# Performance work log

Hardware: AMD Instinct MI355X
Metric: run time of the kernel (lower is better)

The kernel has to match this reference:

```python
import jax, jax.numpy as jnp
import numpy as np

B, D, L, NH = 8, 1024, 1024, 8
DK = D // NH  # = Dv = 128
NEG = -1e30


def setup_inputs() -> dict:
    key = jax.random.key(0)
    kx, km, kq, kk, kv, ko = jax.random.split(key, 6)
    x = jax.random.normal(kx, (B, D, L), dtype=jnp.float32)
    # binary mask over sequence positions (float, as in the torch code)
    mask = (jax.random.uniform(km, (B, L)) > 0.1).astype(jnp.float32)
    # xavier-ish scale for per-head projections, kaiming-ish for Wo
    s_qkv = np.sqrt(2.0 / (D + DK)).astype(np.float32)
    Wq = jax.random.normal(kq, (NH, D, DK), dtype=jnp.float32) * s_qkv
    Wk = jax.random.normal(kk, (NH, D, DK), dtype=jnp.float32) * s_qkv
    Wv = jax.random.normal(kv, (NH, D, DK), dtype=jnp.float32) * s_qkv
    Wo = jax.random.normal(ko, (D, DK * NH), dtype=jnp.float32) * np.sqrt(2.0 / D).astype(np.float32)
    return {"x": x, "mask": mask, "Wq": Wq, "Wk": Wk, "Wv": Wv, "Wo": Wo}


def reference(x, mask, Wq, Wk, Wv, Wo):
    # x: [B, D, L] -> [B, L, D]
    xt = jnp.swapaxes(x, 1, 2)
    scale = 1.0 / np.sqrt(DK).astype(np.float32)
    # batched per-head projections (equivalent to the per-head loop)
    q = jnp.einsum("bld,hdk->bhlk", xt, Wq)  # [B,H,L,Dk]
    k = jnp.einsum("bld,hdk->bhlk", xt, Wk)
    v = jnp.einsum("bld,hdk->bhlk", xt, Wv)
    # scores[b,h,q_pos,k_pos]
    scores = jnp.einsum("bhqd,bhkd->bhqk", q, k) * scale
    # mask.unsqueeze(2) in torch -> additive mask along the QUERY axis
    scores = scores + (1.0 - mask)[:, None, :, None] * NEG
    # faithful quirk: softmax over dim=1 of [B,Lq,Lk] == query axis (axis=2 here)
    attn = jax.nn.softmax(scores, axis=2)
    heads = jnp.einsum("bhqk,bhkd->bhqd", attn, v)  # [B,H,L,Dv]
    head = jnp.swapaxes(heads, 1, 2).reshape(B, L, NH * DK)  # concat heads
    out = head @ Wo  # [B, L, D]
    return jnp.swapaxes(out, 1, 2)  # [B, D, L]
```

## Files before the change

### kernel.cpp

```cpp
#include <hip/hip_runtime.h>

typedef short bf16x8 __attribute__((ext_vector_type(8)));
typedef float f32x4 __attribute__((ext_vector_type(4)));

#define MASK_NEG (-1e30f)

__device__ __forceinline__ unsigned short f2bf(float f) {
  union { float f; unsigned u; } v; v.f = f;
  unsigned r = v.u + 0x7fffu + ((v.u >> 16) & 1u);
  return (unsigned short)(r >> 16);
}

__device__ __forceinline__ void gl_lds16(const void* g, void* l) {
  __builtin_amdgcn_global_load_lds(
      (__attribute__((address_space(1))) void*)(void*)g,
      (__attribute__((address_space(3))) void*)l, 16, 0, 0);
}

__device__ __forceinline__ void transpose_tile(
    const float* __restrict__ s, unsigned short* __restrict__ d,
    int R, int C, int x0, int y0, int t, float tile[64][65]) {
  {
    const int r = t >> 4, c4 = (t & 15) * 4;
    for (int it = 0; it < 4; ++it) {
      const int rr = r + it * 16;
      const float4 v = *(const float4*)(s + (size_t)(y0 + rr) * C + x0 + c4);
      tile[rr][c4 + 0] = v.x; tile[rr][c4 + 1] = v.y;
      tile[rr][c4 + 2] = v.z; tile[rr][c4 + 3] = v.w;
    }
  }
  __syncthreads();
  {
    const int cc = t >> 4, r4 = (t & 15) * 4;
    for (int it = 0; it < 4; ++it) {
      const int c = cc + it * 16;
      ushort4 o;
      o.x = f2bf(tile[r4 + 0][c]); o.y = f2bf(tile[r4 + 1][c]);
      o.z = f2bf(tile[r4 + 2][c]); o.w = f2bf(tile[r4 + 3][c]);
      *(ushort4*)(d + (size_t)(x0 + c) * R + y0 + r4) = o;
    }
  }
}

__global__ __launch_bounds__(256) void transpose_x_wo(
    const float* __restrict__ x, const float* __restrict__ Wo,
    unsigned short* __restrict__ xt, unsigned short* __restrict__ Wot) {
  __shared__ float tile[64][65];
  const int z = blockIdx.z;
  const float* s = (z < 8) ? (x + (size_t)z * 1048576) : Wo;
  unsigned short* d = (z < 8) ? (xt + (size_t)z * 1048576) : Wot;
  transpose_tile(s, d, 1024, 1024, blockIdx.x * 64, blockIdx.y * 64,
                 threadIdx.x, tile);
}

__global__ __launch_bounds__(256) void transpose_w24(
    const float* __restrict__ Wq, const float* __restrict__ Wk,
    const float* __restrict__ Wv, unsigned short* __restrict__ WqkvT) {
  __shared__ float tile[64][65];
  const int z = blockIdx.z;
  const int sel = z >> 3, h = z & 7;
  const float* base = (sel == 0) ? Wq : (sel == 1) ? Wk : Wv;
  const float* s = base + (size_t)h * 131072;
  unsigned short* d = WqkvT + (size_t)z * 131072;
  transpose_tile(s, d, 1024, 128, blockIdx.x * 64, blockIdx.y * 64,
                 threadIdx.x, tile);
}

template<bool F32OUT>
__global__ __launch_bounds__(256) void gemm_tn(
    const unsigned short* __restrict__ A, const unsigned short* __restrict__ B,
    void* __restrict__ Cv,
    int K, int ldA, int ldB, int ldC, float scale,
    long sAl, long sAb, long sAh,
    long sBl, long sBb, long sBh,
    long sCl, long sCb, long sCh,
    int zbase, int zdiv, unsigned short* __restrict__ Vt)
{
  __shared__ unsigned short As[128 * 64];
  __shared__ unsigned short Bs[128 * 64];
  int bx, by, bz;
  {
    const int nx = gridDim.x, ny = gridDim.y;
    const int nwg = nx * ny * gridDim.z;
    int flat = blockIdx.x + nx * (blockIdx.y + ny * blockIdx.z);
    if ((nwg & 7) == 0) flat = (flat & 7) * (nwg >> 3) + (flat >> 3);
    bx = flat % nx; flat /= nx;
    by = flat % ny; bz = flat / ny;
  }
  const int z = bz;
  const int g = zbase + z;
  const int gb = g / zdiv, gh = g % zdiv;
  const unsigned short* Ab = A + (size_t)z * sAl + (size_t)gb * sAb + (size_t)gh * sAh;
  const unsigned short* Bb = B + (size_t)z * sBl + (size_t)gb * sBb + (size_t)gh * sBh;
  const int m0 = by * 128, n0 = bx * 128;
  const int t = threadIdx.x;
  const int lane = t & 63;
  const int wave = t >> 6;
  const int wm = wave >> 1, wn = wave & 1;

  const int sr2 = t >> 3;
  const int ss8 = t & 7;
  const int sq8 = ss8 ^ (sr2 & 7);

  const unsigned short* ap0 = Ab + (size_t)(m0 +  0 + sr2) * ldA + sq8 * 8;
  const unsigned short* ap1 = Ab + (size_t)(m0 + 32 + sr2) * ldA + sq8 * 8;
  const unsigned short* ap2 = Ab + (size_t)(m0 + 64 + sr2) * ldA + sq8 * 8;
  const unsigned short* ap3 = Ab + (size_t)(m0 + 96 + sr2) * ldA + sq8 * 8;
  const unsigned short* bp0 = Bb + (size_t)(n0 +  0 + sr2) * ldB + sq8 * 8;
  const unsigned short* bp1 = Bb + (size_t)(n0 + 32 + sr2) * ldB + sq8 * 8;
  const unsigned short* bp2 = Bb + (size_t)(n0 + 64 + sr2) * ldB + sq8 * 8;
  const unsigned short* bp3 = Bb + (size_t)(n0 + 96 + sr2) * ldB + sq8 * 8;

  char* asd0 = (char*)As +     0 + t * 16;
  char* asd1 = (char*)As +  4096 + t * 16;
  char* asd2 = (char*)As +  8192 + t * 16;
  char* asd3 = (char*)As + 12288 + t * 16;
  char* bsd0 = (char*)Bs +     0 + t * 16;
  char* bsd1 = (char*)Bs +  4096 + t * 16;
  char* bsd2 = (char*)Bs +  8192 + t * 16;
  char* bsd3 = (char*)Bs + 12288 + t * 16;

  const int tq = lane & 15, qd = lane >> 4;

  f32x4 acc[4][4];
  #pragma unroll
  for (int i = 0; i < 4; ++i)
    #pragma unroll
    for (int j = 0; j < 4; ++j)
      acc[i][j] = f32x4{0.f, 0.f, 0.f, 0.f};

  const int kIters = K >> 6;
  for (int kt = 0; kt < kIters; ++kt) {
    __syncthreads();
    gl_lds16(ap0, asd0); gl_lds16(ap1, asd1);
    gl_lds16(ap2, asd2); gl_lds16(ap3, asd3);
    gl_lds16(bp0, bsd0); gl_lds16(bp1, bsd1);
    gl_lds16(bp2, bsd2); gl_lds16(bp3, bsd3);
    ap0 += 64; ap1 += 64; ap2 += 64; ap3 += 64;
    bp0 += 64; bp1 += 64; bp2 += 64; bp3 += 64;
    __builtin_amdgcn_s_waitcnt(0x0f70);
    __syncthreads();

    #pragma unroll
    for (int kk = 0; kk < 2; ++kk) {
      bf16x8 af[4], bfr[4];
      #pragma unroll
      for (int i = 0; i < 4; ++i) {
        const int R = wm * 64 + i * 16 + tq;
        const int slot = (kk * 4 + qd) ^ (R & 7);
        af[i] = *(const bf16x8*)(As + R * 64 + slot * 8);
      }
      #pragma unroll
      for (int j = 0; j < 4; ++j) {
        const int R = wn * 64 + j * 16 + tq;
        const int slot = (kk * 4 + qd) ^ (R & 7);
        bfr[j] = *(const bf16x8*)(Bs + R * 64 + slot * 8);
      }
      #pragma unroll
      for (int i = 0; i < 4; ++i)
        #pragma unroll
        for (int j = 0; j < 4; ++j)
          acc[i][j] = __builtin_amdgcn_mfma_f32_16x16x32_bf16(af[i], bfr[j], acc[i][j], 0, 0, 0);
    }
  }

  if (!F32OUT && Vt != nullptr && gh >= 16) {
    unsigned short* Vb = Vt + (size_t)(gb * 8 + (gh - 16)) * 131072;
    #pragma unroll
    for (int i = 0; i < 4; ++i) {
      const int row = m0 + wm * 64 + i * 16 + qd * 4;
      #pragma unroll
      for (int j = 0; j < 4; ++j) {
        const int col = n0 + wn * 64 + j * 16 + tq;
        ushort4 o;
        o.x = f2bf(acc[i][j][0] * scale);
        o.y = f2bf(acc[i][j][1] * scale);
        o.z = f2bf(acc[i][j][2] * scale);
        o.w = f2bf(acc[i][j][3] * scale);
        *(ushort4*)(Vb + (size_t)col * 1024 + row) = o;
      }
    }
    return;
  }

  const size_t cOff = (size_t)z * sCl + (size_t)gb * sCb + (size_t)gh * sCh;
  #pragma unroll
  for (int i = 0; i < 4; ++i) {
    const int row = m0 + wm * 64 + i * 16 + qd * 4;
    #pragma unroll
    for (int j = 0; j < 4; ++j) {
      const int col = n0 + wn * 64 + j * 16 + tq;
      if constexpr (F32OUT) {
        float* C = (float*)Cv + cOff;
        #pragma unroll
        for (int rr = 0; rr < 4; ++rr)
          C[(size_t)(row + rr) * ldC + col] = acc[i][j][rr] * scale;
      } else {
        unsigned short* C = (unsigned short*)Cv + cOff;
        #pragma unroll
        for (int rr = 0; rr < 4; ++rr)
          C[(size_t)(row + rr) * ldC + col] = f2bf(acc[i][j][rr] * scale);
      }
    }
  }
}

__global__ __launch_bounds__(256, 2) void scores_colsum(
    const unsigned short* __restrict__ QKV, float* __restrict__ colsum,
    const float* __restrict__ mask)
{
  __shared__ unsigned short lds[24576];
  unsigned short* Qs = lds;

  const int bid = blockIdx.x;
  const int w = ((bid & 7) << 6) | (bid >> 3);
  const int g = w >> 3, qx = w & 7;
  const int b = g >> 3, h = g & 7;
  const unsigned short* Qg = QKV + (size_t)b * 3145728 + (size_t)h * 131072
                                 + (size_t)qx * 16384;
  const unsigned short* Kg = QKV + (size_t)b * 3145728 + (size_t)(8 + h) * 131072;

  const int t = threadIdx.x;
  const int lane = t & 63, wave = t >> 6;
  const int wm = wave >> 1, wn = wave & 1;
  const int tq = lane & 15, qd = lane >> 4;

  #pragma unroll
  for (int it = 0; it < 8; ++it) {
    const int c = it * 256 + t;
    const int row = c >> 4;
    const int src = (c ^ (c >> 4)) & 15;
    gl_lds16(Qg + (size_t)row * 128 + src * 8, (char*)Qs + c * 16);
  }
  #pragma unroll
  for (int it = 0; it < 4; ++it) {
    const int c = it * 256 + t;
    const int row = c >> 4;
    const int src = (c ^ (c >> 4)) & 15;
    gl_lds16(Kg + (size_t)row * 128 + src * 8, (char*)(lds + 16384) + c * 16);
  }
  __builtin_amdgcn_s_waitcnt(0x0f70);
  __syncthreads();

  bf16x8 qf[4][4];
  #pragma unroll
  for (int i = 0; i < 4; ++i) {
    const int R = wm * 64 + i * 16 + tq;
    #pragma unroll
    for (int kk = 0; kk < 4; ++kk)
      qf[i][kk] = *(const bf16x8*)(Qs + R * 128 + (((kk * 4 + qd) ^ (R & 15)) * 8));
  }
  __syncthreads();

  const float scl = 0.08838834764831845f;
  float aq[4][4];
  {
    const float* mrow = mask + (size_t)b * 1024 + qx * 128;
    #pragma unroll
    for (int i = 0; i < 4; ++i) {
      const float4 m4 = *(const float4*)(mrow + wm * 64 + i * 16 + qd * 4);
      aq[i][0] = (1.f - m4.x) * MASK_NEG - 20.f;
      aq[i][1] = (1.f - m4.y) * MASK_NEG - 20.f;
      aq[i][2] = (1.f - m4.z) * MASK_NEG - 20.f;
      aq[i][3] = (1.f - m4.w) * MASK_NEG - 20.f;
    }
  }
  float* cs = colsum + (size_t)g * 1024;

  for (int kt = 0; kt < 16; ++kt) {
    __syncthreads();
    if (kt < 15) {
      unsigned short* Kn = ((kt + 1) & 1) ? lds : (lds + 16384);
      const unsigned short* Kgn = Kg + (size_t)(kt + 1) * 64 * 128;
      #pragma unroll
      for (int it = 0; it < 4; ++it) {
        const int c = it * 256 + t;
        const int row = c >> 4;
        const int src = (c ^ (c >> 4)) & 15;
        gl_lds16(Kgn + (size_t)row * 128 + src * 8, (char*)Kn + c * 16);
      }
      __builtin_amdgcn_s_waitcnt(0x0f74);
    } else {
      __builtin_amdgcn_s_waitcnt(0x0f70);
    }
    __syncthreads();

    const unsigned short* Kc = (kt & 1) ? lds : (lds + 16384);
    f32x4 acc_s[4][2];
    #pragma unroll
    for (int i = 0; i < 4; ++i)
      #pragma unroll
      for (int j = 0; j < 2; ++j)
        acc_s[i][j] = f32x4{0.f, 0.f, 0.f, 0.f};
    #pragma unroll
    for (int kk = 0; kk < 4; ++kk) {
      bf16x8 kf[2];
      #pragma unroll
      for (int j = 0; j < 2; ++j) {
        const int R = wn * 32 + j * 16 + tq;
        kf[j] = *(const bf16x8*)(Kc + R * 128 + (((kk * 4 + qd) ^ (R & 15)) * 8));
      }
      #pragma unroll
      for (int i = 0; i < 4; ++i)
        #pragma unroll
        for (int j = 0; j < 2; ++j)
          acc_s[i][j] = __builtin_amdgcn_mfma_f32_16x16x32_bf16(qf[i][kk], kf[j], acc_s[i][j], 0, 0, 0);
    }

    float cp0 = 0.f, cp1 = 0.f;
    #pragma unroll
    for (int i = 0; i < 4; ++i)
      #pragma unroll
      for (int rr = 0; rr < 4; ++rr) {
        cp0 += __expf(acc_s[i][0][rr] * scl + aq[i][rr]);
        cp1 += __expf(acc_s[i][1][rr] * scl + aq[i][rr]);
      }
    cp0 += __shfl_xor(cp0, 16, 64); cp0 += __shfl_xor(cp0, 32, 64);
    cp1 += __shfl_xor(cp1, 16, 64); cp1 += __shfl_xor(cp1, 32, 64);
    if (qd == 0) {
      atomicAdd(&cs[kt * 64 + wn * 32 + tq], cp0);
      atomicAdd(&cs[kt * 64 + wn * 32 + 16 + tq], cp1);
    }
  }
}

__global__ __launch_bounds__(256, 2) void attn_pv_fused(
    const unsigned short* __restrict__ QKV, const unsigned short* __restrict__ Vp,
    unsigned short* __restrict__ Hp, const float* __restrict__ mask,
    const float* __restrict__ colsum)
{
  __shared__ unsigned short lds[40960];
  unsigned short* Ps = lds;
  unsigned short* Qs = lds;

  const int bid = blockIdx.x;
  const int w = ((bid & 7) << 6) | (bid >> 3);
  const int g = w >> 3, qx = w & 7;
  const int b = g >> 3, h = g & 7;
  const unsigned short* Qg = QKV + (size_t)b * 3145728 + (size_t)h * 131072
                                 + (size_t)qx * 16384;
  const unsigned short* Kg = QKV + (size_t)b * 3145728 + (size_t)(8 + h) * 131072;
  const unsigned short* Vg = Vp + (size_t)g * 131072;

  const int t = threadIdx.x;
  const int lane = t & 63, wave = t >> 6;
  const int wm = wave >> 1, wn = wave & 1;
  const int tq = lane & 15, qd = lane >> 4;

  #pragma unroll
  for (int it = 0; it < 8; ++it) {
    const int c = it * 256 + t;
    const int row = c >> 4;
    const int src = (c ^ (c >> 4)) & 15;
    gl_lds16(Qg + (size_t)row * 128 + src * 8, (char*)Qs + c * 16);
  }
  #pragma unroll
  for (int it = 0; it < 4; ++it) {
    const int c = it * 256 + t;
    const int row = c >> 4;
    const int src = (c ^ (c >> 4)) & 15;
    gl_lds16(Kg + (size_t)row * 128 + src * 8, (char*)(lds + 16384) + c * 16);
  }
  #pragma unroll
  for (int it = 0; it < 4; ++it) {
    const int c = it * 256 + t;
    const int row = c >> 3;
    const int src = (c ^ (c >> 3)) & 7;
    gl_lds16(Vg + (size_t)row * 1024 + src * 8, (char*)(lds + 24576) + c * 16);
  }
  __builtin_amdgcn_s_waitcnt(0x0f70);
  __syncthreads();

  bf16x8 qf[4][4];
  #pragma unroll
  for (int i = 0; i < 4; ++i) {
    const int R = wm * 64 + i * 16 + tq;
    #pragma unroll
    for (int kk = 0; kk < 4; ++kk)
      qf[i][kk] = *(const bf16x8*)(Qs + R * 128 + (((kk * 4 + qd) ^ (R & 15)) * 8));
  }
  __syncthreads();

  f32x4 acc_h[4][4];
  #pragma unroll
  for (int i = 0; i < 4; ++i)
    #pragma unroll
    for (int j = 0; j < 4; ++j)
      acc_h[i][j] = f32x4{0.f, 0.f, 0.f, 0.f};

  const float scl = 0.08838834764831845f;
  float aq[4][4];
  {
    const float* mrow = mask + (size_t)b * 1024 + qx * 128;
    #pragma unroll
    for (int i = 0; i < 4; ++i) {
      const float4 m4 = *(const float4*)(mrow + wm * 64 + i * 16 + qd * 4);
      aq[i][0] = (1.f - m4.x) * MASK_NEG - 20.f;
      aq[i][1] = (1.f - m4.y) * MASK_NEG - 20.f;
      aq[i][2] = (1.f - m4.z) * MASK_NEG - 20.f;
      aq[i][3] = (1.f - m4.w) * MASK_NEG - 20.f;
    }
  }
  const float* cs = colsum + (size_t)g * 1024;

  for (int kt = 0; kt < 16; ++kt) {
    __syncthreads();
    if (kt < 15) {
      unsigned short* Kn = ((kt + 1) & 1) ? (lds + 8192) : (lds + 16384);
      unsigned short* Vn = ((kt + 1) & 1) ? (lds + 32768) : (lds + 24576);
      const unsigned short* Kgn = Kg + (size_t)(kt + 1) * 64 * 128;
      #pragma unroll
      for (int it = 0; it < 4; ++it) {
        const int c = it * 256 + t;
        const int row = c >> 4;
        const int src = (c ^ (c >> 4)) & 15;
        gl_lds16(Kgn + (size_t)row * 128 + src * 8, (char*)Kn + c * 16);
      }
      #pragma unroll
      for (int it = 0; it < 4; ++it) {
        const int c = it * 256 + t;
        const int row = c >> 3;
        const int src = (c ^ (c >> 3)) & 7;
        gl_lds16(Vg + (size_t)row * 1024 + (kt + 1) * 64 + src * 8, (char*)Vn + c * 16);
      }
      __builtin_amdgcn_s_waitcnt(0x0f78);
    } else {
      __builtin_amdgcn_s_waitcnt(0x0f70);
    }
    __syncthreads();

    const unsigned short* Kc = (kt & 1) ? (lds + 8192) : (lds + 16384);
    const unsigned short* Vc = (kt & 1) ? (lds + 32768) : (lds + 24576);

    f32x4 acc_s[4][2];
    #pragma unroll
    for (int i = 0; i < 4; ++i)
      #pragma unroll
      for (int j = 0; j < 2; ++j)
        acc_s[i][j] = f32x4{0.f, 0.f, 0.f, 0.f};
    #pragma unroll
    for (int kk = 0; kk < 4; ++kk) {
      bf16x8 kf[2];
      #pragma unroll
      for (int j = 0; j < 2; ++j) {
        const int R = wn * 32 + j * 16 + tq;
        kf[j] = *(const bf16x8*)(Kc + R * 128 + (((kk * 4 + qd) ^ (R & 15)) * 8));
      }
      #pragma unroll
      for (int i = 0; i < 4; ++i)
        #pragma unroll
        for (int j = 0; j < 2; ++j)
          acc_s[i][j] = __builtin_amdgcn_mfma_f32_16x16x32_bf16(qf[i][kk], kf[j], acc_s[i][j], 0, 0, 0);
    }

    const float rcs0 = 1.0f / cs[kt * 64 + wn * 32 + tq];
    const float rcs1 = 1.0f / cs[kt * 64 + wn * 32 + 16 + tq];
    #pragma unroll
    for (int i = 0; i < 4; ++i) {
      const int q0 = wm * 64 + i * 16 + qd * 4;
      #pragma unroll
      for (int rr = 0; rr < 4; ++rr) {
        const int q = q0 + rr;
        #pragma unroll
        for (int j = 0; j < 2; ++j) {
          const int kl = wn * 32 + j * 16 + tq;
          const float e = __expf(acc_s[i][j][rr] * scl + aq[i][rr]) * (j ? rcs1 : rcs0);
          Ps[q * 64 + ((((kl >> 3) ^ (q & 7)) * 8) | (kl & 7))] = f2bf(e);
        }
      }
    }
    __syncthreads();

    #pragma unroll
    for (int k2 = 0; k2 < 2; ++k2) {
      bf16x8 pf[4], vf[4];
      #pragma unroll
      for (int i = 0; i < 4; ++i) {
        const int R = wm * 64 + i * 16 + tq;
        pf[i] = *(const bf16x8*)(Ps + R * 64 + (((k2 * 4 + qd) ^ (R & 7)) * 8));
      }
      #pragma unroll
      for (int j = 0; j < 4; ++j) {
        const int R = wn * 64 + j * 16 + tq;
        vf[j] = *(const bf16x8*)(Vc + R * 64 + (((k2 * 4 + qd) ^ (R & 7)) * 8));
      }
      #pragma unroll
      for (int i = 0; i < 4; ++i)
        #pragma unroll
        for (int j = 0; j < 4; ++j)
          acc_h[i][j] = __builtin_amdgcn_mfma_f32_16x16x32_bf16(pf[i], vf[j], acc_h[i][j], 0, 0, 0);
    }
  }

  unsigned short* Hb = Hp + (size_t)b * 1048576 + (size_t)qx * 131072 + h * 128;
  #pragma unroll
  for (int i = 0; i < 4; ++i) {
    const int q0 = wm * 64 + i * 16 + qd * 4;
    #pragma unroll
    for (int j = 0; j < 4; ++j) {
      const int dv = wn * 64 + j * 16 + tq;
      #pragma unroll
      for (int rr = 0; rr < 4; ++rr)
        Hb[(size_t)(q0 + rr) * 1024 + dv] = f2bf(acc_h[i][j][rr]);
    }
  }
}

extern "C" void kernel_launch(void* const* d_in, const int* in_sizes, int n_in,
                              void* d_out, int out_size, void* d_ws, size_t ws_size,
                              hipStream_t stream) {
  const float* x    = (const float*)d_in[0];
  const float* mask = (const float*)d_in[1];
  const float* Wq   = (const float*)d_in[2];
  const float* Wk   = (const float*)d_in[3];
  const float* Wv   = (const float*)d_in[4];
  const float* Wo   = (const float*)d_in[5];
  float* out = (float*)d_out;

  char* p = (char*)d_ws;
  unsigned short* xt    = (unsigned short*)p; p += 16777216;
  unsigned short* WqkvT = (unsigned short*)p; p += 6291456;
  unsigned short* Wot   = (unsigned short*)p; p += 2097152;
  unsigned short* QKV   = (unsigned short*)p; p += 50331648;
  unsigned short* Vp    = (unsigned short*)p; p += 16777216;
  unsigned short* Hp    = (unsigned short*)p; p += 16777216;
  float* colsum = (float*)p; p += 262144;

  hipMemsetAsync(colsum, 0, 262144, stream);

  transpose_x_wo<<<dim3(16, 16, 9), 256, 0, stream>>>(x, Wo, xt, Wot);
  transpose_w24<<<dim3(2, 16, 24), 256, 0, stream>>>(Wq, Wk, Wv, WqkvT);

  gemm_tn<false><<<dim3(1, 8, 192), 256, 0, stream>>>(
      xt, WqkvT, (void*)QKV, 1024, 1024, 1024, 128, 1.f,
      0L, 1048576L, 0L,  0L, 0L, 131072L,  0L, 3145728L, 131072L, 0, 24, Vp);

  scores_colsum<<<dim3(512, 1, 1), 256, 0, stream>>>(QKV, colsum, mask);

  attn_pv_fused<<<dim3(512, 1, 1), 256, 0, stream>>>(QKV, Vp, Hp, mask, colsum);

  gemm_tn<true><<<dim3(8, 8, 8), 256, 0, stream>>>(
      Wot, Hp, (void*)out, 1024, 1024, 1024, 1024, 1.f,
      0L, 0L, 0L,  0L, 1048576L, 0L,  0L, 1048576L, 0L, 0, 1, nullptr);
}
```

Baseline: 285.2 us.

## Accumulate column sums in LDS and relax barrier waitcnts for deeper prefetch

In scores_colsum, per-tile column partial sums now go into a shared-memory buffer split by wave row, and each block flushes them with one coalesced atomicAdd pass at the end. This replaces many scattered global atomics issued inside the loop. Both kernels also swap __syncthreads for raw s_barrier plus explicit vmcnt waits, which lets the K/V prefetch for the next tile stay in flight across the barriers instead of draining. The hand-picked vmcnt values must match the number of outstanding loads exactly, so a miscount could read LDS before the data arrives.

```diff
diff --git a/kernel.cpp b/kernel.cpp
--- a/kernel.cpp
+++ b/kernel.cpp
@@ -210,6 +210,7 @@
     const float* __restrict__ mask)
 {
   __shared__ unsigned short lds[24576];
+  __shared__ float csacc[2][1024];
   unsigned short* Qs = lds;
 
   const int bid = blockIdx.x;
@@ -265,13 +266,12 @@
       aq[i][3] = (1.f - m4.w) * MASK_NEG - 20.f;
     }
   }
-  float* cs = colsum + (size_t)g * 1024;
 
   for (int kt = 0; kt < 16; ++kt) {
-    __syncthreads();
+    __builtin_amdgcn_s_barrier();
     if (kt < 15) {
       unsigned short* Kn = ((kt + 1) & 1) ? lds : (lds + 16384);
-      const unsigned short* Kgn = Kg + (size_t)(kt + 1) * 64 * 128;
+      const unsigned short* Kgn = Kg + (size_t)(kt + 1) * 8192;
       #pragma unroll
       for (int it = 0; it < 4; ++it) {
         const int c = it * 256 + t;
@@ -279,11 +279,11 @@
         const int src = (c ^ (c >> 4)) & 15;
         gl_lds16(Kgn + (size_t)row * 128 + src * 8, (char*)Kn + c * 16);
       }
-      __builtin_amdgcn_s_waitcnt(0x0f74);
+      asm volatile("s_waitcnt vmcnt(4)" ::: "memory");
     } else {
-      __builtin_amdgcn_s_waitcnt(0x0f70);
-    }
-    __syncthreads();
+      asm volatile("s_waitcnt vmcnt(0)" ::: "memory");
+    }
+    __builtin_amdgcn_s_barrier();
 
     const unsigned short* Kc = (kt & 1) ? lds : (lds + 16384);
     f32x4 acc_s[4][2];
@@ -318,9 +318,17 @@
     cp0 += __shfl_xor(cp0, 16, 64); cp0 += __shfl_xor(cp0, 32, 64);
     cp1 += __shfl_xor(cp1, 16, 64); cp1 += __shfl_xor(cp1, 32, 64);
     if (qd == 0) {
-      atomicAdd(&cs[kt * 64 + wn * 32 + tq], cp0);
-      atomicAdd(&cs[kt * 64 + wn * 32 + 16 + tq], cp1);
-    }
+      csacc[wm][kt * 64 + wn * 32 + tq] = cp0;
+      csacc[wm][kt * 64 + wn * 32 + 16 + tq] = cp1;
+    }
+  }
+
+  __syncthreads();
+  float* cs = colsum + (size_t)g * 1024;
+  #pragma unroll
+  for (int r = 0; r < 4; ++r) {
+    const int idx = r * 256 + t;
+    atomicAdd(&cs[idx], csacc[0][idx] + csacc[1][idx]);
   }
 }
 
@@ -404,11 +412,11 @@
   const float* cs = colsum + (size_t)g * 1024;
 
   for (int kt = 0; kt < 16; ++kt) {
-    __syncthreads();
+    __builtin_amdgcn_s_barrier();
     if (kt < 15) {
       unsigned short* Kn = ((kt + 1) & 1) ? (lds + 8192) : (lds + 16384);
       unsigned short* Vn = ((kt + 1) & 1) ? (lds + 32768) : (lds + 24576);
-      const unsigned short* Kgn = Kg + (size_t)(kt + 1) * 64 * 128;
+      const unsigned short* Kgn = Kg + (size_t)(kt + 1) * 8192;
       #pragma unroll
       for (int it = 0; it < 4; ++it) {
         const int c = it * 256 + t;
@@ -423,11 +431,11 @@
         const int src = (c ^ (c >> 3)) & 7;
         gl_lds16(Vg + (size_t)row * 1024 + (kt + 1) * 64 + src * 8, (char*)Vn + c * 16);
       }
-      __builtin_amdgcn_s_waitcnt(0x0f78);
+      asm volatile("s_waitcnt vmcnt(12)" ::: "memory");
     } else {
-      __builtin_amdgcn_s_waitcnt(0x0f70);
-    }
-    __syncthreads();
+      asm volatile("s_waitcnt vmcnt(4)" ::: "memory");
+    }
+    __builtin_amdgcn_s_barrier();
 
     const unsigned short* Kc = (kt & 1) ? (lds + 8192) : (lds + 16384);
     const unsigned short* Vc = (kt & 1) ? (lds + 32768) : (lds + 24576);
@@ -469,7 +477,11 @@
         }
       }
     }
-    __syncthreads();
+    if (kt < 15)
+      asm volatile("s_waitcnt vmcnt(8) lgkmcnt(0)" ::: "memory");
+    else
+      asm volatile("s_waitcnt vmcnt(0) lgkmcnt(0)" ::: "memory");
+    __builtin_amdgcn_s_barrier();
 
     #pragma unroll
     for (int k2 = 0; k2 < 2; ++k2) {
```

Result: faster. 277.5 us (-2.7%).

## Halve query tile per block, single-buffer K/V, and batch colsum atomics

Applied to the files above, without the earlier changes.

Both attention kernels now process 64 query rows per block instead of 128, launching twice as many blocks with launch bounds raised to 4 blocks per CU. K/V double buffering is dropped in favour of a single LDS buffer to cut LDS and register use. The colsum kernel accumulates per-tile column partials in shared memory and issues one atomic per column at the end instead of atomics every tile. MFMA sections are wrapped in s_setprio. The trade-off is that K/V loads are no longer overlapped with compute within a block, and each block now re-reads the full K (and V) for half as many queries, so that traffic doubles. The bet is that the extra occupancy hides the load latency.

```diff
diff --git a/kernel.cpp b/kernel.cpp
--- a/kernel.cpp
+++ b/kernel.cpp
@@ -205,19 +205,18 @@
   }
 }
 
-__global__ __launch_bounds__(256, 2) void scores_colsum(
+__global__ __launch_bounds__(256, 4) void scores_colsum(
     const unsigned short* __restrict__ QKV, float* __restrict__ colsum,
     const float* __restrict__ mask)
 {
-  __shared__ unsigned short lds[24576];
-  unsigned short* Qs = lds;
-
+  __shared__ unsigned short kbuf[8192];
+  __shared__ float csacc[2][1024];
   const int bid = blockIdx.x;
-  const int w = ((bid & 7) << 6) | (bid >> 3);
-  const int g = w >> 3, qx = w & 7;
+  const int w = ((bid & 7) << 7) | (bid >> 3);
+  const int g = w >> 4, qx = w & 15;
   const int b = g >> 3, h = g & 7;
   const unsigned short* Qg = QKV + (size_t)b * 3145728 + (size_t)h * 131072
-                                 + (size_t)qx * 16384;
+                                 + (size_t)qx * 8192;
   const unsigned short* Kg = QKV + (size_t)b * 3145728 + (size_t)(8 + h) * 131072;
 
   const int t = threadIdx.x;
@@ -226,90 +225,75 @@
   const int tq = lane & 15, qd = lane >> 4;
 
   #pragma unroll
-  for (int it = 0; it < 8; ++it) {
-    const int c = it * 256 + t;
-    const int row = c >> 4;
-    const int src = (c ^ (c >> 4)) & 15;
-    gl_lds16(Qg + (size_t)row * 128 + src * 8, (char*)Qs + c * 16);
-  }
-  #pragma unroll
   for (int it = 0; it < 4; ++it) {
     const int c = it * 256 + t;
     const int row = c >> 4;
     const int src = (c ^ (c >> 4)) & 15;
-    gl_lds16(Kg + (size_t)row * 128 + src * 8, (char*)(lds + 16384) + c * 16);
-  }
-  __builtin_amdgcn_s_waitcnt(0x0f70);
+    gl_lds16(Qg + (size_t)row * 128 + src * 8, (char*)kbuf + c * 16);
+  }
   __syncthreads();
 
-  bf16x8 qf[4][4];
-  #pragma unroll
-  for (int i = 0; i < 4; ++i) {
-    const int R = wm * 64 + i * 16 + tq;
+  bf16x8 qf[2][4];
+  #pragma unroll
+  for (int i = 0; i < 2; ++i) {
+    const int q = wm * 32 + i * 16 + tq;
     #pragma unroll
     for (int kk = 0; kk < 4; ++kk)
-      qf[i][kk] = *(const bf16x8*)(Qs + R * 128 + (((kk * 4 + qd) ^ (R & 15)) * 8));
+      qf[i][kk] = *(const bf16x8*)(kbuf + q * 128 + (((kk * 4 + qd) ^ (q & 15)) * 8));
   }
   __syncthreads();
 
   const float scl = 0.08838834764831845f;
-  float aq[4][4];
+  float aq[2][4];
   {
-    const float* mrow = mask + (size_t)b * 1024 + qx * 128;
-    #pragma unroll
-    for (int i = 0; i < 4; ++i) {
-      const float4 m4 = *(const float4*)(mrow + wm * 64 + i * 16 + qd * 4);
+    const float* mrow = mask + (size_t)b * 1024 + qx * 64;
+    #pragma unroll
+    for (int i = 0; i < 2; ++i) {
+      const float4 m4 = *(const float4*)(mrow + wm * 32 + i * 16 + qd * 4);
       aq[i][0] = (1.f - m4.x) * MASK_NEG - 20.f;
       aq[i][1] = (1.f - m4.y) * MASK_NEG - 20.f;
       aq[i][2] = (1.f - m4.z) * MASK_NEG - 20.f;
       aq[i][3] = (1.f - m4.w) * MASK_NEG - 20.f;
     }
   }
-  float* cs = colsum + (size_t)g * 1024;
 
   for (int kt = 0; kt < 16; ++kt) {
     __syncthreads();
-    if (kt < 15) {
-      unsigned short* Kn = ((kt + 1) & 1) ? lds : (lds + 16384);
-      const unsigned short* Kgn = Kg + (size_t)(kt + 1) * 64 * 128;
-      #pragma unroll
-      for (int it = 0; it < 4; ++it) {
-        const int c = it * 256 + t;
-        const int row = c >> 4;
-        const int src = (c ^ (c >> 4)) & 15;
-        gl_lds16(Kgn + (size_t)row * 128 + src * 8, (char*)Kn + c * 16);
-      }
-      __builtin_amdgcn_s_waitcnt(0x0f74);
-    } else {
-      __builtin_amdgcn_s_waitcnt(0x0f70);
-    }
-    __syncthreads();
-
-    const unsigned short* Kc = (kt & 1) ? lds : (lds + 16384);
-    f32x4 acc_s[4][2];
-    #pragma unroll
-    for (int i = 0; i < 4; ++i)
+    #pragma unroll
+    for (int it = 0; it < 4; ++it) {
+      const int c = it * 256 + t;
+      const int row = c >> 4;
+      const int src = (c ^ (c >> 4)) & 15;
+      gl_lds16(Kg + (size_t)(kt * 64 + row) * 128 + src * 8, (char*)kbuf + c * 16);
+    }
+    __syncthreads();
+
+    f32x4 acc_s[2][2];
+    #pragma unroll
+    for (int i = 0; i < 2; ++i)
       #pragma unroll
       for (int j = 0; j < 2; ++j)
         acc_s[i][j] = f32x4{0.f, 0.f, 0.f, 0.f};
+    __builtin_amdgcn_s_setprio(1);
     #pragma unroll
     for (int kk = 0; kk < 4; ++kk) {
       bf16x8 kf[2];
       #pragma unroll
       for (int j = 0; j < 2; ++j) {
-        const int R = wn * 32 + j * 16 + tq;
-        kf[j] = *(const bf16x8*)(Kc + R * 128 + (((kk * 4 + qd) ^ (R & 15)) * 8));
-      }
-      #pragma unroll
-      for (int i = 0; i < 4; ++i)
+        const int k = wn * 32 + j * 16 + tq;
+        kf[j] = *(const bf16x8*)(kbuf + k * 128 + (((kk * 4 + qd) ^ (k & 15)) * 8));
+      }
+      #pragma unroll
+      for (int i = 0; i < 2; ++i)
         #pragma unroll
         for (int j = 0; j < 2; ++j)
           acc_s[i][j] = __builtin_amdgcn_mfma_f32_16x16x32_bf16(qf[i][kk], kf[j], acc_s[i][j], 0, 0, 0);
     }
+    __builtin_amdgcn_s_setprio(0);
 
     float cp0 = 0.f, cp1 = 0.f;
     #pragma unroll
-    for (int i = 0; i < 4; ++i)
+    for (int i = 0; i < 2; ++i)
       #pragma unroll
       for (int rr = 0; rr < 4; ++rr) {
         cp0 += __expf(acc_s[i][0][rr] * scl + aq[i][rr]);
@@ -318,27 +302,36 @@
     cp0 += __shfl_xor(cp0, 16, 64); cp0 += __shfl_xor(cp0, 32, 64);
     cp1 += __shfl_xor(cp1, 16, 64); cp1 += __shfl_xor(cp1, 32, 64);
     if (qd == 0) {
-      atomicAdd(&cs[kt * 64 + wn * 32 + tq], cp0);
-      atomicAdd(&cs[kt * 64 + wn * 32 + 16 + tq], cp1);
-    }
-  }
-}
-
-__global__ __launch_bounds__(256, 2) void attn_pv_fused(
+      csacc[wm][kt * 64 + wn * 32 + tq] = cp0;
+      csacc[wm][kt * 64 + wn * 32 + 16 + tq] = cp1;
+    }
+  }
+
+  __syncthreads();
+  float* cs = colsum + (size_t)g * 1024;
+  #pragma unroll
+  for (int r = 0; r < 4; ++r) {
+    const int idx = r * 256 + t;
+    atomicAdd(&cs[idx], csacc[0][idx] + csacc[1][idx]);
+  }
+}
+
+__global__ __launch_bounds__(256, 4) void attn_pv_fused(
     const unsigned short* __restrict__ QKV, const unsigned short* __restrict__ Vp,
     unsigned short* __restrict__ Hp, const float* __restrict__ mask,
     const float* __restrict__ colsum)
 {
-  __shared__ unsigned short lds[40960];
+  __shared__ unsigned short lds[20480];
   unsigned short* Ps = lds;
-  unsigned short* Qs = lds;
+  unsigned short* Ks = lds + 4096;
+  unsigned short* Vs = lds + 12288;
 
   const int bid = blockIdx.x;
-  const int w = ((bid & 7) << 6) | (bid >> 3);
-  const int g = w >> 3, qx = w & 7;
+  const int w = ((bid & 7) << 7) | (bid >> 3);
+  const int g = w >> 4, qx = w & 15;
   const int b = g >> 3, h = g & 7;
   const unsigned short* Qg = QKV + (size_t)b * 3145728 + (size_t)h * 131072
-                                 + (size_t)qx * 16384;
+                                 + (size_t)qx * 8192;
   const unsigned short* Kg = QKV + (size_t)b * 3145728 + (size_t)(8 + h) * 131072;
   const unsigned short* Vg = Vp + (size_t)g * 131072;
 
@@ -348,53 +341,38 @@
   const int tq = lane & 15, qd = lane >> 4;
 
   #pragma unroll
-  for (int it = 0; it < 8; ++it) {
-    const int c = it * 256 + t;
-    const int row = c >> 4;
-    const int src = (c ^ (c >> 4)) & 15;
-    gl_lds16(Qg + (size_t)row * 128 + src * 8, (char*)Qs + c * 16);
-  }
-  #pragma unroll
   for (int it = 0; it < 4; ++it) {
     const int c = it * 256 + t;
     const int row = c >> 4;
     const int src = (c ^ (c >> 4)) & 15;
-    gl_lds16(Kg + (size_t)row * 128 + src * 8, (char*)(lds + 16384) + c * 16);
-  }
-  #pragma unroll
-  for (int it = 0; it < 4; ++it) {
-    const int c = it * 256 + t;
-    const int row = c >> 3;
-    const int src = (c ^ (c >> 3)) & 7;
-    gl_lds16(Vg + (size_t)row * 1024 + src * 8, (char*)(lds + 24576) + c * 16);
-  }
-  __builtin_amdgcn_s_waitcnt(0x0f70);
+    gl_lds16(Qg + (size_t)row * 128 + src * 8, (char*)Ks + c * 16);
+  }
   __syncthreads();
 
-  bf16x8 qf[4][4];
-  #pragma unroll
-  for (int i = 0; i < 4; ++i) {
-    const int R = wm * 64 + i * 16 + tq;
+  bf16x8 qf[2][4];
+  #pragma unroll
+  for (int i = 0; i < 2; ++i) {
+    const int q = wm * 32 + i * 16 + tq;
     #pragma unroll
     for (int kk = 0; kk < 4; ++kk)
-      qf[i][kk] = *(const bf16x8*)(Qs + R * 128 + (((kk * 4 + qd) ^ (R & 15)) * 8));
+      qf[i][kk] = *(const bf16x8*)(Ks + q * 128 + (((kk * 4 + qd) ^ (q & 15)) * 8));
   }
   __syncthreads();
 
-  f32x4 acc_h[4][4];
-  #pragma unroll
-  for (int i = 0; i < 4; ++i)
+  f32x4 acc_h[2][4];
+  #pragma unroll
+  for (int i = 0; i < 2; ++i)
     #pragma unroll
     for (int j = 0; j < 4; ++j)
       acc_h[i][j] = f32x4{0.f, 0.f, 0.f, 0.f};
 
   const float scl = 0.08838834764831845f;
-  float aq[4][4];
+  float aq[2][4];
   {
-    const float* mrow = mask + (size_t)b * 1024 + qx * 128;
-    #pragma unroll
-    for (int i = 0; i < 4; ++i) {
-      const float4 m4 = *(const float4*)(mrow + wm * 64 + i * 16 + qd * 4);
+    const float* mrow = mask + (size_t)b * 1024 + qx * 64;
+    #pragma unroll
+    for (int i = 0; i < 2; ++i) {
+      const float4 m4 = *(const float4*)(mrow + wm * 32 + i * 16 + qd * 4);
       aq[i][0] = (1.f - m4.x) * MASK_NEG - 20.f;
       aq[i][1] = (1.f - m4.y) * MASK_NEG - 20.f;
       aq[i][2] = (1.f - m4.z) * MASK_NEG - 20.f;
@@ -405,59 +383,50 @@
 
   for (int kt = 0; kt < 16; ++kt) {
     __syncthreads();
-    if (kt < 15) {
-      unsigned short* Kn = ((kt + 1) & 1) ? (lds + 8192) : (lds + 16384);
-      unsigned short* Vn = ((kt + 1) & 1) ? (lds + 32768) : (lds + 24576);
-      const unsigned short* Kgn = Kg + (size_t)(kt + 1) * 64 * 128;
-      #pragma unroll
-      for (int it = 0; it < 4; ++it) {
-        const int c = it * 256 + t;
-        const int row = c >> 4;
-        const int src = (c ^ (c >> 4)) & 15;
-        gl_lds16(Kgn + (size_t)row * 128 + src * 8, (char*)Kn + c * 16);
-      }
-      #pragma unroll
-      for (int it = 0; it < 4; ++it) {
-        const int c = it * 256 + t;
-        const int row = c >> 3;
-        const int src = (c ^ (c >> 3)) & 7;
-        gl_lds16(Vg + (size_t)row * 1024 + (kt + 1) * 64 + src * 8, (char*)Vn + c * 16);
-      }
-      __builtin_amdgcn_s_waitcnt(0x0f78);
-    } else {
-      __builtin_amdgcn_s_waitcnt(0x0f70);
-    }
-    __syncthreads();
-
-    const unsigned short* Kc = (kt & 1) ? (lds + 8192) : (lds + 16384);
-    const unsigned short* Vc = (kt & 1) ? (lds + 32768) : (lds + 24576);
-
-    f32x4 acc_s[4][2];
-    #pragma unroll
-    for (int i = 0; i < 4; ++i)
+    #pragma unroll
+    for (int it = 0; it < 4; ++it) {
+      const int c = it * 256 + t;
+      const int row = c >> 4;
+      const int src = (c ^ (c >> 4)) & 15;
+      gl_lds16(Kg + (size_t)(kt * 64 + row) * 128 + src * 8, (char*)Ks + c * 16);
+    }
+    #pragma unroll
+    for (int it = 0; it < 4; ++it) {
+      const int c = it * 256 + t;
+      const int row = c >> 3;
+      const int src = (c ^ (c >> 3)) & 7;
+      gl_lds16(Vg + (size_t)row * 1024 + kt * 64 + src * 8, (char*)Vs + c * 16);
+    }
+    const float rcs0 = 1.0f / cs[kt * 64 + wn * 32 + tq];
+    const float rcs1 = 1.0f / cs[kt * 64 + wn * 32 + 16 + tq];
+    __syncthreads();
+
+    f32x4 acc_s[2][2];
+    #pragma unroll
+    for (int i = 0; i < 2; ++i)
       #pragma unroll
       for (int j = 0; j < 2; ++j)
         acc_s[i][j] = f32x4{0.f, 0.f, 0.f, 0.f};
+    __builtin_amdgcn_s_setprio(1);
     #pragma unroll
     for (int kk = 0; kk < 4; ++kk) {
       bf16x8 kf[2];
       #pragma unroll
       for (int j = 0; j < 2; ++j) {
-        const int R = wn * 32 + j * 16 + tq;
-        kf[j] = *(const bf16x8*)(Kc + R * 128 + (((kk * 4 + qd) ^ (R & 15)) * 8));
-      }
-      #pragma unroll
-      for (int i = 0; i < 4; ++i)
+        const int k = wn * 32 + j * 16 + tq;
+        kf[j] = *(const bf16x8*)(Ks + k * 128 + (((kk * 4 + qd) ^ (k & 15)) * 8));
+      }
+      #pragma unroll
+      for (int i = 0; i < 2; ++i)
         #pragma unroll
         for (int j = 0; j < 2; ++j)
           acc_s[i][j] = __builtin_amdgcn_mfma_f32_16x16x32_bf16(qf[i][kk], kf[j], acc_s[i][j], 0, 0, 0);
     }
-
-    const float rcs0 = 1.0f / cs[kt * 64 + wn * 32 + tq];
-    const float rcs1 = 1.0f / cs[kt * 64 + wn * 32 + 16 + tq];
-    #pragma unroll
-    for (int i = 0; i < 4; ++i) {
-      const int q0 = wm * 64 + i * 16 + qd * 4;
+    __builtin_amdgcn_s_setprio(0);
+
+    #pragma unroll
+    for (int i = 0; i < 2; ++i) {
+      const int q0 = wm * 32 + i * 16 + qd * 4;
       #pragma unroll
       for (int rr = 0; rr < 4; ++rr) {
         const int q = q0 + rr;
@@ -465,37 +434,40 @@
         for (int j = 0; j < 2; ++j) {
           const int kl = wn * 32 + j * 16 + tq;
           const float e = __expf(acc_s[i][j][rr] * scl + aq[i][rr]) * (j ? rcs1 : rcs0);
-          Ps[q * 64 + ((((kl >> 3) ^ (q & 7)) * 8) | (kl & 7))] = f2bf(e);
+          Ps[q * 64 + (((kl >> 3) ^ (q & 7)) * 8) + (kl & 7)] = f2bf(e);
         }
       }
     }
     __syncthreads();
 
+    __builtin_amdgcn_s_setprio(1);
     #pragma unroll
     for (int k2 = 0; k2 < 2; ++k2) {
-      bf16x8 pf[4], vf[4];
-      #pragma unroll
-      for (int i = 0; i < 4; ++i) {
-        const int R = wm * 64 + i * 16 + tq;
-        pf[i] = *(const bf16x8*)(Ps + R * 64 + (((k2 * 4 + qd) ^ (R & 7)) * 8));
+      const int o = k2 * 4 + qd;
+      bf16x8 pf[2], vf[4];
+      #pragma unroll
+      for (int i = 0; i < 2; ++i) {
+        const int q = wm * 32 + i * 16 + tq;
+        pf[i] = *(const bf16x8*)(Ps + q * 64 + ((o ^ (q & 7)) * 8));
       }
       #pragma unroll
       for (int j = 0; j < 4; ++j) {
-        const int R = wn * 64 + j * 16 + tq;
-        vf[j] = *(const bf16x8*)(Vc + R * 64 + (((k2 * 4 + qd) ^ (R & 7)) * 8));
-      }
-      #pragma unroll
-      for (int i = 0; i < 4; ++i)
+        const int dv = wn * 64 + j * 16 + tq;
+        vf[j] = *(const bf16x8*)(Vs + dv * 64 + ((o ^ (dv & 7)) * 8));
+      }
+      #pragma unroll
+      for (int i = 0; i < 2; ++i)
         #pragma unroll
         for (int j = 0; j < 4; ++j)
           acc_h[i][j] = __builtin_amdgcn_mfma_f32_16x16x32_bf16(pf[i], vf[j], acc_h[i][j], 0, 0, 0);
     }
-  }
-
-  unsigned short* Hb = Hp + (size_t)b * 1048576 + (size_t)qx * 131072 + h * 128;
-  #pragma unroll
-  for (int i = 0; i < 4; ++i) {
-    const int q0 = wm * 64 + i * 16 + qd * 4;
+    __builtin_amdgcn_s_setprio(0);
+  }
+
+  unsigned short* Hb = Hp + (size_t)b * 1048576 + (size_t)qx * 65536 + h * 128;
+  #pragma unroll
+  for (int i = 0; i < 2; ++i) {
+    const int q0 = wm * 32 + i * 16 + qd * 4;
     #pragma unroll
     for (int j = 0; j < 4; ++j) {
       const int dv = wn * 64 + j * 16 + tq;
@@ -535,9 +507,9 @@
       xt, WqkvT, (void*)QKV, 1024, 1024, 1024, 128, 1.f,
       0L, 1048576L, 0L,  0L, 0L, 131072L,  0L, 3145728L, 131072L, 0, 24, Vp);
 
-  scores_colsum<<<dim3(512, 1, 1), 256, 0, stream>>>(QKV, colsum, mask);
-
-  attn_pv_fused<<<dim3(512, 1, 1), 256, 0, stream>>>(QKV, Vp, Hp, mask, colsum);
+  scores_colsum<<<dim3(1024, 1, 1), 256, 0, stream>>>(QKV, colsum, mask);
+
+  attn_pv_fused<<<dim3(1024, 1, 1), 256, 0, stream>>>(QKV, Vp, Hp, mask, colsum);
 
   gemm_tn<true><<<dim3(8, 8, 8), 256, 0, stream>>>(
       Wot, Hp, (void*)out, 1024, 1024, 1024, 1024, 1.f,
```

Result: slower. 345.2 us (+21.0%).
